# Kernel optimization log

Hardware: AMD Instinct MI355X
Metric: run time of the kernel (lower is better)

Reference implementation:

```python
import jax, jax.numpy as jnp
import numpy as np

EPS = 1e-5

def _ln(x, w, b):
    m = jnp.mean(x, -1, keepdims=True)
    v = jnp.mean((x - m) ** 2, -1, keepdims=True)
    return (x - m) * jax.lax.rsqrt(v + EPS) * w + b

def _silu(x):
    return x * jax.nn.sigmoid(x)

def _mamba(x, in_proj_w, conv_w, conv_b, x_proj_w, dt_proj_w, dt_proj_b, A_log, D, out_proj_w):
    # x: [Bc, L, d_model]; standard mamba_ssm Mamba block math
    Bc, L, _ = x.shape
    d_inner = conv_b.shape[0]
    d_state = A_log.shape[1]
    dt_rank = dt_proj_w.shape[0]
    xz = x @ in_proj_w                          # [Bc, L, 2*d_inner]
    xm, z = jnp.split(xz, 2, axis=-1)
    # causal depthwise conv1d (pad left d_conv-1, truncate to L)
    xm_t = jnp.transpose(xm, (0, 2, 1))         # [Bc, d_inner, L]
    xm_t = jax.lax.conv_general_dilated(
        xm_t, conv_w[:, None, :], (1,), [(conv_w.shape[-1] - 1, 0)],
        dimension_numbers=('NCH', 'OIH', 'NCH'), feature_group_count=d_inner)
    xm = _silu(jnp.transpose(xm_t, (0, 2, 1)) + conv_b)   # [Bc, L, d_inner]
    x_dbl = xm @ x_proj_w                        # [Bc, L, dt_rank + 2*d_state]
    dt_r = x_dbl[..., :dt_rank]
    Bm = x_dbl[..., dt_rank:dt_rank + d_state]
    Cm = x_dbl[..., dt_rank + d_state:]
    dt = jax.nn.softplus(dt_r @ dt_proj_w + dt_proj_b)    # [Bc, L, d_inner]
    A = -jnp.exp(A_log)                          # [d_inner, d_state]

    def step(h, inp):
        xt, dtt, Bt, Ct = inp                    # [Bc,d_inner],[Bc,d_inner],[Bc,d_state],[Bc,d_state]
        dA = jnp.exp(dtt[:, :, None] * A)
        h = dA * h + (dtt * xt)[:, :, None] * Bt[:, None, :]
        y = jnp.einsum('bds,bs->bd', h, Ct)
        return h, y

    h0 = jnp.zeros((Bc, d_inner, d_state), x.dtype)
    xs = (jnp.transpose(xm, (1, 0, 2)), jnp.transpose(dt, (1, 0, 2)),
          jnp.transpose(Bm, (1, 0, 2)), jnp.transpose(Cm, (1, 0, 2)))
    _, ys = jax.lax.scan(step, h0, xs)
    y = jnp.transpose(ys, (1, 0, 2)) + xm * D    # [Bc, L, d_inner]
    y = y * _silu(z)
    return y @ out_proj_w                        # [Bc, L, d_model]

def _pvmamba(x, ln_w, ln_b, skip_scale, proj_w, proj_b, mp):
    # x: [B, H, W, C]; 4 channel-chunks share one Mamba -> batch them as lanes
    B, H, W, C = x.shape
    n = H * W
    d = C // 4
    xf = x.reshape(B, n, C)
    xn = _ln(xf, ln_w, ln_b)
    xc = jnp.transpose(xn.reshape(B, n, 4, d), (2, 0, 1, 3)).reshape(4 * B, n, d)
    ym = _mamba(xc, *mp) + skip_scale * xc
    ym = jnp.transpose(ym.reshape(4, B, n, d), (1, 2, 0, 3)).reshape(B, n, C)
    ym = _ln(ym, ln_w, ln_b)                     # second LN reuses same params (as in source)
    out = ym @ proj_w + proj_b
    return out.reshape(B, H, W, -1)

def _down(x, w):
    # Conv2d k=2 s=2 no bias, exact non-overlapping patch contraction; w: [O, I, 2, 2]
    B, H, W, C = x.shape
    xr = jnp.transpose(x, (0, 3, 1, 2)).reshape(B, C, H // 2, 2, W // 2, 2)
    y = jnp.einsum('bcipjq,ocpq->boij', xr, w)
    return jnp.transpose(y, (0, 2, 3, 1))

def _up(x, w):
    # ConvTranspose2d k=2 s=2 no bias; w: [I, O, 2, 2] (torch layout)
    B, H, W, C = x.shape
    xc = jnp.transpose(x, (0, 3, 1, 2))
    y = jnp.einsum('bcij,copq->boipjq', xc, w).reshape(B, w.shape[1], 2 * H, 2 * W)
    return jnp.transpose(y, (0, 2, 3, 1))

def _mpma(x, ln_w, ln_b, skip_scale, proj_w, proj_b, in_proj_w, conv_w, conv_b,
          x_proj_w, dt_proj_w, dt_proj_b, A_log, D, out_proj_w, down_w, up_w):
    mp = (in_proj_w, conv_w, conv_b, x_proj_w, dt_proj_w, dt_proj_b, A_log, D, out_proj_w)
    xh = jnp.transpose(x, (0, 2, 3, 1))          # NCHW -> NHWC
    outs = [_pvmamba(xh, ln_w, ln_b, skip_scale, proj_w, proj_b, mp)]
    xin = xh
    for _ in range(1, 5):
        xin = _down(xin, down_w)
        outs.append(_pvmamba(xin, ln_w, ln_b, skip_scale, proj_w, proj_b, mp))
    res = outs[-1]
    for l, od in enumerate(outs[-2::-1]):
        res = od + (1.0 / (l + 1)) * _up(res, up_w)
    return jnp.transpose(res, (0, 3, 2, 1))      # note: (0,3,2,1) as in source -> [B,C,W,H]

def setup_inputs() -> dict:
    B, C, HW = 8, 64, 128
    d_model, d_inner, d_state, d_conv, dt_rank = 16, 32, 16, 4, 1
    key = jax.random.key(0)
    ks = jax.random.split(key, 10)
    x = jax.random.normal(ks[0], (B, C, HW, HW), jnp.float32)
    return {
        'x': x,
        'ln_w': jnp.ones((C,), jnp.float32),
        'ln_b': jnp.zeros((C,), jnp.float32),
        'skip_scale': jnp.ones((1,), jnp.float32),
        'proj_w': jax.random.normal(ks[1], (C, C), jnp.float32) * 0.05,
        'proj_b': jnp.zeros((C,), jnp.float32),
        'in_proj_w': jax.random.normal(ks[2], (d_model, 2 * d_inner), jnp.float32) * 0.1,
        'conv_w': jax.random.normal(ks[3], (d_inner, d_conv), jnp.float32) * 0.2,
        'conv_b': jnp.zeros((d_inner,), jnp.float32),
        'x_proj_w': jax.random.normal(ks[4], (d_inner, dt_rank + 2 * d_state), jnp.float32) * 0.1,
        'dt_proj_w': jax.random.normal(ks[5], (dt_rank, d_inner), jnp.float32) * 0.5,
        'dt_proj_b': jnp.full((d_inner,), -4.0, jnp.float32),
        'A_log': jnp.broadcast_to(jnp.log(jnp.arange(1, d_state + 1, dtype=jnp.float32)), (d_inner, d_state)),
        'D': jnp.ones((d_inner,), jnp.float32),
        'out_proj_w': jax.random.normal(ks[6], (d_inner, d_model), jnp.float32) * 0.1,
        'down_w': jax.random.normal(ks[7], (C, C, 2, 2), jnp.float32) * 0.05,
        'up_w': jax.random.normal(ks[8], (C, C, 2, 2), jnp.float32) * 0.05,
    }

def reference(x, ln_w, ln_b, skip_scale, proj_w, proj_b, in_proj_w, conv_w, conv_b,
              x_proj_w, dt_proj_w, dt_proj_b, A_log, D, out_proj_w, down_w, up_w):
    return _mpma(x, ln_w, ln_b, skip_scale, proj_w, proj_b, in_proj_w, conv_w, conv_b,
                 x_proj_w, dt_proj_w, dt_proj_b, A_log, D, out_proj_w, down_w, up_w)
```

## Files before the change

kernel.cpp:

```cpp
#include <hip/hip_runtime.h>
#include <hip/hip_fp16.h>

#define TMAX 128

__device__ __forceinline__ float silu_f(float x) {
    return x / (1.f + __expf(-x));
}
__device__ __forceinline__ float softplus_f(float x) {
    return (x > 20.f) ? x : log1pf(__expf(x));
}

__global__ __launch_bounds__(256) void k_tr_in(const float* __restrict__ x, float* __restrict__ xh) {
    __shared__ float tile[128 * 65];
    int h = blockIdx.x, b = blockIdx.y;
    const float* ip = x + (size_t)b * 64 * 16384 + (size_t)h * 128;
    for (int i = threadIdx.x; i < 64 * 128; i += 256) {
        int c = i >> 7, w = i & 127;
        tile[w * 65 + c] = ip[(size_t)c * 16384 + w];
    }
    __syncthreads();
    float* op = xh + ((size_t)(b * 128 + h)) * 128 * 64;
    for (int i = threadIdx.x; i < 128 * 64; i += 256) {
        int w = i >> 6, c = i & 63;
        op[i] = tile[w * 65 + c];
    }
}

__global__ __launch_bounds__(256) void k_tr_out(const float* __restrict__ res, float* __restrict__ out) {
    __shared__ float tile[64 * 129];
    int w = blockIdx.x, b = blockIdx.y;
    const float* ip = res + (size_t)b * 16384 * 64 + (size_t)w * 64;
    for (int i = threadIdx.x; i < 128 * 64; i += 256) {
        int h = i >> 6, c = i & 63;
        tile[c * 129 + h] = ip[(size_t)h * 128 * 64 + c];
    }
    __syncthreads();
    float* op = out + (size_t)b * 64 * 16384 + (size_t)w * 128;
    for (int i = threadIdx.x; i < 64 * 128; i += 256) {
        int c = i >> 7, hh = i & 127;
        op[(size_t)c * 16384 + hh] = tile[c * 129 + hh];
    }
}

__global__ __launch_bounds__(256) void k_down(const float* __restrict__ in, float* __restrict__ out,
                                              const float* __restrict__ dwp, int Ho, int Wo, int ntot) {
    __shared__ float dw[16384];
    for (int i = threadIdx.x; i < 16384; i += 256) {
        int o = i & 63, cpq = i >> 6;
        dw[cpq * 64 + o] = dwp[o * 256 + cpq];
    }
    __syncthreads();
    int gid = blockIdx.x * 256 + threadIdx.x;
    if (gid >= ntot) return;
    int og = gid & 3, pix = gid >> 2;
    int j = pix % Wo, i2 = (pix / Wo) % Ho, b = pix / (Wo * Ho);
    const float* ip = in + (((size_t)b * (2 * Ho) + 2 * i2) * (size_t)(2 * Wo) + 2 * j) * 64;
    float acc[16];
#pragma unroll
    for (int m = 0; m < 16; ++m) acc[m] = 0.f;
    for (int p = 0; p < 2; ++p) {
        for (int q = 0; q < 2; ++q) {
            const float* xp = ip + ((size_t)p * (2 * Wo) + q) * 64;
            for (int c = 0; c < 64; ++c) {
                float xv = xp[c];
                const float* wrow = &dw[(c * 4 + p * 2 + q) * 64 + og * 16];
#pragma unroll
                for (int m = 0; m < 16; ++m) acc[m] = fmaf(xv, wrow[m], acc[m]);
            }
        }
    }
    float* op = out + (size_t)pix * 64 + og * 16;
#pragma unroll
    for (int m = 0; m < 4; ++m) {
        float4 v = make_float4(acc[m * 4], acc[m * 4 + 1], acc[m * 4 + 2], acc[m * 4 + 3]);
        *(float4*)(op + m * 4) = v;
    }
}

__global__ __launch_bounds__(256) void k_up(const float* __restrict__ src, float* __restrict__ dst,
                                            const float* __restrict__ uwp, int H, int W, float coef, int ntot) {
    __shared__ float uw[16384];
    for (int i = threadIdx.x; i < 16384; i += 256) {
        int o = i & 63, cpq = i >> 6;
        int c = cpq >> 2, pq = cpq & 3;
        uw[cpq * 64 + o] = uwp[c * 256 + o * 4 + pq];
    }
    __syncthreads();
    int gid = blockIdx.x * 256 + threadIdx.x;
    if (gid >= ntot) return;
    int og = gid & 3, pix = gid >> 2;
    int x = pix % W, y = (pix / W) % H, b = pix / (W * H);
    int Hs = H >> 1, Ws = W >> 1;
    int pq = (y & 1) * 2 + (x & 1);
    const float* sp = src + (((size_t)b * Hs + (y >> 1)) * (size_t)Ws + (x >> 1)) * 64;
    float acc[16];
#pragma unroll
    for (int m = 0; m < 16; ++m) acc[m] = 0.f;
    for (int c = 0; c < 64; ++c) {
        float xv = sp[c];
        const float* wrow = &uw[(c * 4 + pq) * 64 + og * 16];
#pragma unroll
        for (int m = 0; m < 16; ++m) acc[m] = fmaf(xv, wrow[m], acc[m]);
    }
    float* op = dst + (size_t)pix * 64 + og * 16;
#pragma unroll
    for (int m = 0; m < 4; ++m) {
        float4 cur = *(float4*)(op + m * 4);
        cur.x += coef * acc[m * 4];
        cur.y += coef * acc[m * 4 + 1];
        cur.z += coef * acc[m * 4 + 2];
        cur.w += coef * acc[m * 4 + 3];
        *(float4*)(op + m * 4) = cur;
    }
}

__global__ __launch_bounds__(256) void k_pre(const float* __restrict__ xh, __half2* __restrict__ stream,
                                             const float* __restrict__ lnw, const float* __restrict__ lnb,
                                             const float* __restrict__ in_proj_w, const float* __restrict__ conv_w,
                                             const float* __restrict__ conv_b, const float* __restrict__ x_proj_w,
                                             const float* __restrict__ dt_w, const float* __restrict__ dt_b,
                                             int n, int nseq, int seq_base) {
    __shared__ float pre[259][33];
    __shared__ float Wm[16][32];
    __shared__ float Wxp[32][33];
    __shared__ float cw[32][4];
    __shared__ float cb[32], dtw[32], dtb[32];
    __shared__ float lw[64], lb[64];
    const int tid = threadIdx.x;
    const int t0 = blockIdx.x * 256;
    const int seqL = blockIdx.y;
    const int seqG = seq_base + seqL;
    const int b = seqG >> 2, g = seqG & 3;

    for (int i = tid; i < 512; i += 256) Wm[i >> 5][i & 31] = in_proj_w[(i >> 5) * 64 + (i & 31)];
    for (int i = tid; i < 32 * 33; i += 256) Wxp[i / 33][i % 33] = x_proj_w[i];
    for (int i = tid; i < 128; i += 256) cw[i >> 2][i & 3] = conv_w[i];
    if (tid < 32) { cb[tid] = conv_b[tid]; dtw[tid] = dt_w[tid]; dtb[tid] = dt_b[tid]; }
    if (tid < 64) { lw[tid] = lnw[tid]; lb[tid] = lnb[tid]; }
    __syncthreads();

    const int Tcb = min(256, n - t0);
    const int rows = Tcb + 3;
    for (int r = tid; r < rows; r += 256) {
        int t = t0 + r - 3;
        if (t < 0) {
#pragma unroll
            for (int d = 0; d < 32; ++d) pre[r][d] = 0.f;
        } else {
            const float4* xp = (const float4*)(xh + ((size_t)b * n + t) * 64);
            float4 v[16];
            float s = 0.f;
#pragma unroll
            for (int i = 0; i < 16; ++i) { v[i] = xp[i]; s += v[i].x + v[i].y + v[i].z + v[i].w; }
            float m = s * (1.f / 64.f);
            float q = 0.f;
#pragma unroll
            for (int i = 0; i < 16; ++i) {
                float a = v[i].x - m, b2 = v[i].y - m, c = v[i].z - m, dd = v[i].w - m;
                q += a * a + b2 * b2 + c * c + dd * dd;
            }
            float rr = rsqrtf(q * (1.f / 64.f) + 1e-5f);
            const float4* xg = (const float4*)(xh + ((size_t)b * n + t) * 64 + g * 16);
            float xn16[16];
#pragma unroll
            for (int i = 0; i < 4; ++i) {
                float4 u4 = xg[i];
                int c0 = g * 16 + i * 4;
                xn16[i * 4 + 0] = (u4.x - m) * rr * lw[c0 + 0] + lb[c0 + 0];
                xn16[i * 4 + 1] = (u4.y - m) * rr * lw[c0 + 1] + lb[c0 + 1];
                xn16[i * 4 + 2] = (u4.z - m) * rr * lw[c0 + 2] + lb[c0 + 2];
                xn16[i * 4 + 3] = (u4.w - m) * rr * lw[c0 + 3] + lb[c0 + 3];
            }
#pragma unroll
            for (int d = 0; d < 32; ++d) {
                float a = 0.f;
#pragma unroll
                for (int j = 0; j < 16; ++j) a = fmaf(xn16[j], Wm[j][d], a);
                pre[r][d] = a;
            }
        }
    }
    __syncthreads();

    if (tid < Tcb) {
        const int t = t0 + tid;
        float xmv[32];
#pragma unroll
        for (int d = 0; d < 32; ++d) {
            float a = cb[d];
#pragma unroll
            for (int k = 0; k < 4; ++k) a = fmaf(pre[tid + k][d], cw[d][k], a);
            xmv[d] = silu_f(a);
        }
        float dtr = 0.f;
#pragma unroll
        for (int d = 0; d < 32; ++d) dtr = fmaf(xmv[d], Wxp[d][0], dtr);
        const size_t sb = (size_t)seqL * n + t;
#pragma unroll
        for (int d = 0; d < 32; ++d) {
            float dtv = softplus_f(fmaf(dtr, dtw[d], dtb[d]));
            stream[(size_t)d * nseq * n + sb] = __floats2half2_rn(dtv, xmv[d]);
        }
#pragma unroll
        for (int p = 0; p < 8; ++p) {
            float b0 = 0.f, b1 = 0.f;
#pragma unroll
            for (int d = 0; d < 32; ++d) {
                b0 = fmaf(xmv[d], Wxp[d][1 + 2 * p], b0);
                b1 = fmaf(xmv[d], Wxp[d][2 + 2 * p], b1);
            }
            stream[(size_t)(32 + p) * nseq * n + sb] = __floats2half2_rn(b0, b1);
        }
#pragma unroll
        for (int p = 0; p < 8; ++p) {
            float c0 = 0.f, c1 = 0.f;
#pragma unroll
            for (int d = 0; d < 32; ++d) {
                c0 = fmaf(xmv[d], Wxp[d][17 + 2 * p], c0);
                c1 = fmaf(xmv[d], Wxp[d][18 + 2 * p], c1);
            }
            stream[(size_t)(40 + p) * nseq * n + sb] = __floats2half2_rn(c0, c1);
        }
    }
}

__global__ __launch_bounds__(256) void k_scanA(const __half2* __restrict__ stream, float* __restrict__ P,
                                               float* __restrict__ H, const float* __restrict__ A_log,
                                               int n, int nseq, int nch) {
    const int tid = threadIdx.x;
    const int d = tid >> 3, ss = tid & 7;
    const int chunk = blockIdx.x, seqL = blockIdx.y;
    const int t0 = chunk * TMAX;
    const int Tc = min(TMAX, n - t0);
    const float a0 = -__expf(A_log[d * 16 + 2 * ss]);
    const float a1 = -__expf(A_log[d * 16 + 2 * ss + 1]);
    const __half2* pdx = stream + ((size_t)d * nseq + seqL) * n + t0;
    const __half2* pB = stream + ((size_t)(32 + ss) * nseq + seqL) * n + t0;
    float h0 = 0.f, h1 = 0.f, sdt = 0.f;
    for (int t = 0; t < Tc; ++t) {
        float2 dx = __half22float2(pdx[t]);
        float2 bv = __half22float2(pB[t]);
        float u = dx.x * dx.y;
        h0 = fmaf(__expf(a0 * dx.x), h0, u * bv.x);
        h1 = fmaf(__expf(a1 * dx.x), h1, u * bv.y);
        sdt += dx.x;
    }
    const size_t cbi = ((size_t)seqL * nch + chunk) * 512 + tid * 2;
    *(float2*)&P[cbi] = make_float2(__expf(a0 * sdt), __expf(a1 * sdt));
    *(float2*)&H[cbi] = make_float2(h0, h1);
}

__global__ __launch_bounds__(256) void k_scanB(const float* __restrict__ P, const float* __restrict__ Hl,
                                               float* __restrict__ hin, int nch, int nseq) {
    int idx = blockIdx.x * 256 + threadIdx.x;
    if (idx >= nseq * 512) return;
    int seq = idx >> 9, ds = idx & 511;
    size_t base = (size_t)seq * nch * 512 + ds;
    float h = 0.f;
    for (int k = 0; k < nch; ++k) {
        hin[base + (size_t)k * 512] = h;
        h = fmaf(P[base + (size_t)k * 512], h, Hl[base + (size_t)k * 512]);
    }
}

__global__ __launch_bounds__(256) void k_scanC(const __half2* __restrict__ stream, const float* __restrict__ hin,
                                               const float* __restrict__ xh, float* __restrict__ ym,
                                               const float* __restrict__ A_log,
                                               const float* __restrict__ lnw, const float* __restrict__ lnb,
                                               const float* __restrict__ in_proj_w, const float* __restrict__ Dvec,
                                               const float* __restrict__ out_proj_w,
                                               const float* __restrict__ skip_scale,
                                               int n, int nseq, int seq_base, int nch) {
    __shared__ float yb[TMAX][33];
    __shared__ float Wz[16][32];
    __shared__ float Wout[32][16];
    __shared__ float lw[64], lb[64];
    __shared__ float Dsh[32];
    const int tid = threadIdx.x;
    const int d = tid >> 3, ss = tid & 7;
    const int chunk = blockIdx.x, seqL = blockIdx.y;
    const int seqG = seq_base + seqL;
    const int b = seqG >> 2, g = seqG & 3;
    const int t0 = chunk * TMAX;
    const int Tc = min(TMAX, n - t0);

    for (int i = tid; i < 512; i += 256) Wz[i >> 5][i & 31] = in_proj_w[(i >> 5) * 64 + 32 + (i & 31)];
    for (int i = tid; i < 512; i += 256) Wout[i >> 4][i & 15] = out_proj_w[i];
    if (tid < 64) { lw[tid] = lnw[tid]; lb[tid] = lnb[tid]; }
    if (tid < 32) Dsh[tid] = Dvec[tid];

    const float a0 = -__expf(A_log[d * 16 + 2 * ss]);
    const float a1 = -__expf(A_log[d * 16 + 2 * ss + 1]);
    const __half2* pdx = stream + ((size_t)d * nseq + seqL) * n + t0;
    const __half2* pB = stream + ((size_t)(32 + ss) * nseq + seqL) * n + t0;
    const __half2* pC = stream + ((size_t)(40 + ss) * nseq + seqL) * n + t0;
    const size_t cbi = ((size_t)seqL * nch + chunk) * 512 + tid * 2;
    float2 hi2 = *(const float2*)&hin[cbi];
    float h0 = hi2.x, h1 = hi2.y;

    for (int t = 0; t < Tc; ++t) {
        float2 dx = __half22float2(pdx[t]);
        float2 bv = __half22float2(pB[t]);
        float2 cv = __half22float2(pC[t]);
        float u = dx.x * dx.y;
        h0 = fmaf(__expf(a0 * dx.x), h0, u * bv.x);
        h1 = fmaf(__expf(a1 * dx.x), h1, u * bv.y);
        float pp = fmaf(h0, cv.x, h1 * cv.y);
        pp += __shfl_xor(pp, 1);
        pp += __shfl_xor(pp, 2);
        pp += __shfl_xor(pp, 4);
        if (ss == 0) yb[t][d] = pp;
    }
    __syncthreads();

    if (tid < Tc) {
        const int t = t0 + tid;
        const float4* xp = (const float4*)(xh + ((size_t)b * n + t) * 64);
        float4 v[16];
        float s = 0.f;
#pragma unroll
        for (int i = 0; i < 16; ++i) { v[i] = xp[i]; s += v[i].x + v[i].y + v[i].z + v[i].w; }
        float m = s * (1.f / 64.f);
        float q = 0.f;
#pragma unroll
        for (int i = 0; i < 16; ++i) {
            float a = v[i].x - m, b2 = v[i].y - m, c = v[i].z - m, dd = v[i].w - m;
            q += a * a + b2 * b2 + c * c + dd * dd;
        }
        float rr = rsqrtf(q * (1.f / 64.f) + 1e-5f);
        const float4* xg = (const float4*)(xh + ((size_t)b * n + t) * 64 + g * 16);
        float xc[16];
#pragma unroll
        for (int i = 0; i < 4; ++i) {
            float4 u4 = xg[i];
            int c0 = g * 16 + i * 4;
            xc[i * 4 + 0] = (u4.x - m) * rr * lw[c0 + 0] + lb[c0 + 0];
            xc[i * 4 + 1] = (u4.y - m) * rr * lw[c0 + 1] + lb[c0 + 1];
            xc[i * 4 + 2] = (u4.z - m) * rr * lw[c0 + 2] + lb[c0 + 2];
            xc[i * 4 + 3] = (u4.w - m) * rr * lw[c0 + 3] + lb[c0 + 3];
        }
        float yv[32];
#pragma unroll
        for (int dd = 0; dd < 32; ++dd) {
            float2 dx = __half22float2(stream[((size_t)dd * nseq + seqL) * n + t0 + tid]);
            float zz = 0.f;
#pragma unroll
            for (int j = 0; j < 16; ++j) zz = fmaf(xc[j], Wz[j][dd], zz);
            yv[dd] = (yb[tid][dd] + dx.y * Dsh[dd]) * silu_f(zz);
        }
        float sscale = skip_scale[0];
        float* ymtok = ym + ((size_t)b * n + t) * 64 + g * 16;
#pragma unroll
        for (int jq = 0; jq < 4; ++jq) {
            float o0 = 0.f, o1 = 0.f, o2 = 0.f, o3 = 0.f;
#pragma unroll
            for (int dd = 0; dd < 32; ++dd) {
                o0 = fmaf(yv[dd], Wout[dd][jq * 4 + 0], o0);
                o1 = fmaf(yv[dd], Wout[dd][jq * 4 + 1], o1);
                o2 = fmaf(yv[dd], Wout[dd][jq * 4 + 2], o2);
                o3 = fmaf(yv[dd], Wout[dd][jq * 4 + 3], o3);
            }
            float4 ov = make_float4(o0 + sscale * xc[jq * 4 + 0], o1 + sscale * xc[jq * 4 + 1],
                                    o2 + sscale * xc[jq * 4 + 2], o3 + sscale * xc[jq * 4 + 3]);
            *(float4*)(ymtok + jq * 4) = ov;
        }
    }
}

__global__ __launch_bounds__(256) void k_post(const float* __restrict__ ym, float* __restrict__ outl,
                                              const float* __restrict__ lnw, const float* __restrict__ lnb,
                                              const float* __restrict__ proj_w, const float* __restrict__ proj_b,
                                              int ntok) {
    __shared__ float pw[4096];
    __shared__ float pb[64];
    __shared__ float lw[64], lb[64];
    for (int i = threadIdx.x; i < 4096; i += 256) pw[i] = proj_w[i];
    if (threadIdx.x < 64) {
        pb[threadIdx.x] = proj_b[threadIdx.x];
        lw[threadIdx.x] = lnw[threadIdx.x];
        lb[threadIdx.x] = lnb[threadIdx.x];
    }
    __syncthreads();
    int t = blockIdx.x * 256 + threadIdx.x;
    if (t >= ntok) return;
    const float4* p = (const float4*)(ym + (size_t)t * 64);
    float4 v[16];
    float s = 0.f;
#pragma unroll
    for (int i = 0; i < 16; ++i) {
        v[i] = p[i];
        s += v[i].x + v[i].y + v[i].z + v[i].w;
    }
    float m = s * (1.f / 64.f);
    float q = 0.f;
#pragma unroll
    for (int i = 0; i < 16; ++i) {
        float a = v[i].x - m, b2 = v[i].y - m, c = v[i].z - m, d = v[i].w - m;
        q += a * a + b2 * b2 + c * c + d * d;
    }
    float r = rsqrtf(q * (1.f / 64.f) + 1e-5f);
    float* op = outl + (size_t)t * 64;
    for (int half = 0; half < 2; ++half) {
        float acc[32];
#pragma unroll
        for (int o = 0; o < 32; ++o) acc[o] = pb[half * 32 + o];
#pragma unroll
        for (int i = 0; i < 16; ++i) {
            float vals[4] = {v[i].x, v[i].y, v[i].z, v[i].w};
#pragma unroll
            for (int k = 0; k < 4; ++k) {
                int c = i * 4 + k;
                float vn = (vals[k] - m) * r * lw[c] + lb[c];
                const float* wrow = &pw[c * 64 + half * 32];
#pragma unroll
                for (int o = 0; o < 32; ++o) acc[o] = fmaf(vn, wrow[o], acc[o]);
            }
        }
#pragma unroll
        for (int mq = 0; mq < 8; ++mq) {
            float4 ov = make_float4(acc[mq * 4], acc[mq * 4 + 1], acc[mq * 4 + 2], acc[mq * 4 + 3]);
            *(float4*)(op + half * 32 + mq * 4) = ov;
        }
    }
}

extern "C" void kernel_launch(void* const* d_in, const int* in_sizes, int n_in,
                              void* d_out, int out_size, void* d_ws, size_t ws_size,
                              hipStream_t stream_) {
    (void)in_sizes; (void)n_in; (void)out_size;
    const float* x          = (const float*)d_in[0];
    const float* ln_w       = (const float*)d_in[1];
    const float* ln_b       = (const float*)d_in[2];
    const float* skip_scale = (const float*)d_in[3];
    const float* proj_w     = (const float*)d_in[4];
    const float* proj_b     = (const float*)d_in[5];
    const float* in_proj_w  = (const float*)d_in[6];
    const float* conv_w     = (const float*)d_in[7];
    const float* conv_b     = (const float*)d_in[8];
    const float* x_proj_w   = (const float*)d_in[9];
    const float* dt_proj_w  = (const float*)d_in[10];
    const float* dt_proj_b  = (const float*)d_in[11];
    const float* A_log      = (const float*)d_in[12];
    const float* Dv         = (const float*)d_in[13];
    const float* out_proj_w = (const float*)d_in[14];
    const float* down_w     = (const float*)d_in[15];
    const float* up_w       = (const float*)d_in[16];
    float* out = (float*)d_out;
    float* ws = (float*)d_ws;

    static const int nl[5] = {16384, 4096, 1024, 256, 64};
    static const size_t off_xh[5] = {0, 8388608, 10485760, 11010048, 11141120};
    const size_t OFF_YM = 11173888;
    static const size_t off_out[5] = {19562496, 27951104, 30048256, 30572544, 30703616};
    const size_t OFF_P = 30736384, OFF_H = 32833536, OFF_HIN = 34930688;
    const size_t STR_BYTE_OFF = 37027840ULL * 4ULL;
    __half2* strm = (__half2*)((char*)d_ws + STR_BYTE_OFF);

    k_tr_in<<<dim3(128, 8), dim3(256), 0, stream_>>>(x, ws + off_xh[0]);

    for (int l = 0; l < 4; ++l) {
        int Ho = 128 >> (l + 1);
        int ntot = 8 * Ho * Ho * 4;
        k_down<<<dim3((ntot + 255) / 256), dim3(256), 0, stream_>>>(ws + off_xh[l], ws + off_xh[l + 1],
                                                                    down_w, Ho, Ho, ntot);
    }

    for (int l = 0; l < 5; ++l) {
        int n = nl[l];
        int ntok = 8 * n;
        int nch = (n + TMAX - 1) / TMAX;
        int nblk = (n + 255) / 256;
        int Sl = 1;
        while (Sl < 32 && STR_BYTE_OFF + (size_t)192 * (32 / Sl) * n > ws_size) Sl <<= 1;
        int nseq = 32 / Sl;
        for (int sp = 0; sp < Sl; ++sp) {
            int sb = sp * nseq;
            k_pre<<<dim3(nblk, nseq), dim3(256), 0, stream_>>>(ws + off_xh[l], strm, ln_w, ln_b, in_proj_w,
                                                               conv_w, conv_b, x_proj_w, dt_proj_w, dt_proj_b,
                                                               n, nseq, sb);
            k_scanA<<<dim3(nch, nseq), dim3(256), 0, stream_>>>(strm, ws + OFF_P, ws + OFF_H, A_log, n, nseq, nch);
            k_scanB<<<dim3(nseq * 2), dim3(256), 0, stream_>>>(ws + OFF_P, ws + OFF_H, ws + OFF_HIN, nch, nseq);
            k_scanC<<<dim3(nch, nseq), dim3(256), 0, stream_>>>(strm, ws + OFF_HIN, ws + off_xh[l], ws + OFF_YM,
                                                                A_log, ln_w, ln_b, in_proj_w, Dv, out_proj_w,
                                                                skip_scale, n, nseq, sb, nch);
        }
        k_post<<<dim3((ntok + 255) / 256), dim3(256), 0, stream_>>>(ws + OFF_YM, ws + off_out[l], ln_w, ln_b,
                                                                    proj_w, proj_b, ntok);
    }

    static const float coefs[4] = {1.f, 0.5f, 1.f / 3.f, 0.25f};
    for (int k = 0; k < 4; ++k) {
        int l = 3 - k;
        int H = 128 >> l;
        int ntot = 8 * H * H * 4;
        k_up<<<dim3((ntot + 255) / 256), dim3(256), 0, stream_>>>(ws + off_out[l + 1], ws + off_out[l],
                                                                  up_w, H, H, coefs[k], ntot);
    }

    k_tr_out<<<dim3(128, 8), dim3(256), 0, stream_>>>(ws + off_out[0], out);
}
```

Before: 1.654 ms.

## Switch scan stream to token-major records and remap scan threads per sequence

```diff
diff --git a/kernel.cpp b/kernel.cpp
--- a/kernel.cpp
+++ b/kernel.cpp
@@ -1,7 +1,7 @@
 #include <hip/hip_runtime.h>
 #include <hip/hip_fp16.h>
 
-#define TMAX 128
+#define TCH 64
 
 __device__ __forceinline__ float silu_f(float x) {
     return x / (1.f + __expf(-x));
@@ -114,7 +114,7 @@
     }
 }
 
-__global__ __launch_bounds__(256) void k_pre(const float* __restrict__ xh, __half2* __restrict__ stream,
+__global__ __launch_bounds__(256) void k_pre(const float* __restrict__ xh, char* __restrict__ stream,
                                              const float* __restrict__ lnw, const float* __restrict__ lnb,
                                              const float* __restrict__ in_proj_w, const float* __restrict__ conv_w,
                                              const float* __restrict__ conv_b, const float* __restrict__ x_proj_w,
@@ -160,11 +160,10 @@
                 q += a * a + b2 * b2 + c * c + dd * dd;
             }
             float rr = rsqrtf(q * (1.f / 64.f) + 1e-5f);
-            const float4* xg = (const float4*)(xh + ((size_t)b * n + t) * 64 + g * 16);
             float xn16[16];
 #pragma unroll
             for (int i = 0; i < 4; ++i) {
-                float4 u4 = xg[i];
+                float4 u4 = xp[g * 4 + i];
                 int c0 = g * 16 + i * 4;
                 xn16[i * 4 + 0] = (u4.x - m) * rr * lw[c0 + 0] + lb[c0 + 0];
                 xn16[i * 4 + 1] = (u4.y - m) * rr * lw[c0 + 1] + lb[c0 + 1];
@@ -195,11 +194,11 @@
         float dtr = 0.f;
 #pragma unroll
         for (int d = 0; d < 32; ++d) dtr = fmaf(xmv[d], Wxp[d][0], dtr);
-        const size_t sb = (size_t)seqL * n + t;
+        __half2 hbuf[48];
 #pragma unroll
         for (int d = 0; d < 32; ++d) {
             float dtv = softplus_f(fmaf(dtr, dtw[d], dtb[d]));
-            stream[(size_t)d * nseq * n + sb] = __floats2half2_rn(dtv, xmv[d]);
+            hbuf[d] = __floats2half2_rn(dtv, xmv[d]);
         }
 #pragma unroll
         for (int p = 0; p < 8; ++p) {
@@ -209,7 +208,7 @@
                 b0 = fmaf(xmv[d], Wxp[d][1 + 2 * p], b0);
                 b1 = fmaf(xmv[d], Wxp[d][2 + 2 * p], b1);
             }
-            stream[(size_t)(32 + p) * nseq * n + sb] = __floats2half2_rn(b0, b1);
+            hbuf[32 + p] = __floats2half2_rn(b0, b1);
         }
 #pragma unroll
         for (int p = 0; p < 8; ++p) {
@@ -219,35 +218,52 @@
                 c0 = fmaf(xmv[d], Wxp[d][17 + 2 * p], c0);
                 c1 = fmaf(xmv[d], Wxp[d][18 + 2 * p], c1);
             }
-            stream[(size_t)(40 + p) * nseq * n + sb] = __floats2half2_rn(c0, c1);
-        }
-    }
-}
-
-__global__ __launch_bounds__(256) void k_scanA(const __half2* __restrict__ stream, float* __restrict__ P,
+            hbuf[40 + p] = __floats2half2_rn(c0, c1);
+        }
+        float4* o = (float4*)(stream + ((size_t)seqL * n + t) * 192);
+        const float4* src = (const float4*)hbuf;
+#pragma unroll
+        for (int i = 0; i < 12; ++i) o[i] = src[i];
+    }
+}
+
+__global__ __launch_bounds__(256) void k_scanA(const char* __restrict__ stream, float* __restrict__ P,
                                                float* __restrict__ H, const float* __restrict__ A_log,
                                                int n, int nseq, int nch) {
     const int tid = threadIdx.x;
-    const int d = tid >> 3, ss = tid & 7;
-    const int chunk = blockIdx.x, seqL = blockIdx.y;
-    const int t0 = chunk * TMAX;
-    const int Tc = min(TMAX, n - t0);
-    const float a0 = -__expf(A_log[d * 16 + 2 * ss]);
-    const float a1 = -__expf(A_log[d * 16 + 2 * ss + 1]);
-    const __half2* pdx = stream + ((size_t)d * nseq + seqL) * n + t0;
-    const __half2* pB = stream + ((size_t)(32 + ss) * nseq + seqL) * n + t0;
-    float h0 = 0.f, h1 = 0.f, sdt = 0.f;
-    for (int t = 0; t < Tc; ++t) {
-        float2 dx = __half22float2(pdx[t]);
-        float2 bv = __half22float2(pB[t]);
+    const int wv = tid >> 6, lane = tid & 63;
+    const int d = lane & 31, hh = lane >> 5;
+    const int chunk = blockIdx.x;
+    const int seqL = blockIdx.y * 4 + wv;
+    if (seqL >= nseq) return;
+    const char* rec = stream + ((size_t)seqL * n + (size_t)chunk * TCH) * 192;
+    float Av[8];
+#pragma unroll
+    for (int j = 0; j < 8; ++j) Av[j] = -__expf(A_log[d * 16 + hh * 8 + j]);
+    float hs[8] = {0.f, 0.f, 0.f, 0.f, 0.f, 0.f, 0.f, 0.f};
+    float sdt = 0.f;
+    for (int t = 0; t < TCH; ++t) {
+        const char* r = rec + t * 192;
+        float2 dx = __half22float2(*(const __half2*)(r + d * 4));
+        float4 bv4 = *(const float4*)(r + 128 + hh * 16);
+        const __half2* bh = (const __half2*)&bv4;
         float u = dx.x * dx.y;
-        h0 = fmaf(__expf(a0 * dx.x), h0, u * bv.x);
-        h1 = fmaf(__expf(a1 * dx.x), h1, u * bv.y);
+#pragma unroll
+        for (int j = 0; j < 4; ++j) {
+            float2 bf = __half22float2(bh[j]);
+            hs[2 * j]     = fmaf(__expf(Av[2 * j] * dx.x),     hs[2 * j],     u * bf.x);
+            hs[2 * j + 1] = fmaf(__expf(Av[2 * j + 1] * dx.x), hs[2 * j + 1], u * bf.y);
+        }
         sdt += dx.x;
     }
-    const size_t cbi = ((size_t)seqL * nch + chunk) * 512 + tid * 2;
-    *(float2*)&P[cbi] = make_float2(__expf(a0 * sdt), __expf(a1 * sdt));
-    *(float2*)&H[cbi] = make_float2(h0, h1);
+    size_t base = ((size_t)seqL * nch + chunk) * 512 + d * 16 + hh * 8;
+    float pv[8];
+#pragma unroll
+    for (int j = 0; j < 8; ++j) pv[j] = __expf(Av[j] * sdt);
+    *(float4*)&P[base]     = *(float4*)&pv[0];
+    *(float4*)&P[base + 4] = *(float4*)&pv[4];
+    *(float4*)&H[base]     = *(float4*)&hs[0];
+    *(float4*)&H[base + 4] = *(float4*)&hs[4];
 }
 
 __global__ __launch_bounds__(256) void k_scanB(const float* __restrict__ P, const float* __restrict__ Hl,
@@ -263,7 +279,7 @@
     }
 }
 
-__global__ __launch_bounds__(256) void k_scanC(const __half2* __restrict__ stream, const float* __restrict__ hin,
+__global__ __launch_bounds__(256) void k_scanC(const char* __restrict__ stream, const float* __restrict__ hin,
                                                const float* __restrict__ xh, float* __restrict__ ym,
                                                const float* __restrict__ A_log,
                                                const float* __restrict__ lnw, const float* __restrict__ lnb,
@@ -271,50 +287,61 @@
                                                const float* __restrict__ out_proj_w,
                                                const float* __restrict__ skip_scale,
                                                int n, int nseq, int seq_base, int nch) {
-    __shared__ float yb[TMAX][33];
+    __shared__ float yb[4][TCH][33];
     __shared__ float Wz[16][32];
     __shared__ float Wout[32][16];
     __shared__ float lw[64], lb[64];
-    __shared__ float Dsh[32];
     const int tid = threadIdx.x;
-    const int d = tid >> 3, ss = tid & 7;
-    const int chunk = blockIdx.x, seqL = blockIdx.y;
-    const int seqG = seq_base + seqL;
-    const int b = seqG >> 2, g = seqG & 3;
-    const int t0 = chunk * TMAX;
-    const int Tc = min(TMAX, n - t0);
-
     for (int i = tid; i < 512; i += 256) Wz[i >> 5][i & 31] = in_proj_w[(i >> 5) * 64 + 32 + (i & 31)];
     for (int i = tid; i < 512; i += 256) Wout[i >> 4][i & 15] = out_proj_w[i];
     if (tid < 64) { lw[tid] = lnw[tid]; lb[tid] = lnb[tid]; }
-    if (tid < 32) Dsh[tid] = Dvec[tid];
-
-    const float a0 = -__expf(A_log[d * 16 + 2 * ss]);
-    const float a1 = -__expf(A_log[d * 16 + 2 * ss + 1]);
-    const __half2* pdx = stream + ((size_t)d * nseq + seqL) * n + t0;
-    const __half2* pB = stream + ((size_t)(32 + ss) * nseq + seqL) * n + t0;
-    const __half2* pC = stream + ((size_t)(40 + ss) * nseq + seqL) * n + t0;
-    const size_t cbi = ((size_t)seqL * nch + chunk) * 512 + tid * 2;
-    float2 hi2 = *(const float2*)&hin[cbi];
-    float h0 = hi2.x, h1 = hi2.y;
-
-    for (int t = 0; t < Tc; ++t) {
-        float2 dx = __half22float2(pdx[t]);
-        float2 bv = __half22float2(pB[t]);
-        float2 cv = __half22float2(pC[t]);
-        float u = dx.x * dx.y;
-        h0 = fmaf(__expf(a0 * dx.x), h0, u * bv.x);
-        h1 = fmaf(__expf(a1 * dx.x), h1, u * bv.y);
-        float pp = fmaf(h0, cv.x, h1 * cv.y);
-        pp += __shfl_xor(pp, 1);
-        pp += __shfl_xor(pp, 2);
-        pp += __shfl_xor(pp, 4);
-        if (ss == 0) yb[t][d] = pp;
-    }
-    __syncthreads();
-
-    if (tid < Tc) {
-        const int t = t0 + tid;
+    __syncthreads();
+
+    const int wv = tid >> 6, lane = tid & 63;
+    const int d = lane & 31, hh = lane >> 5;
+    const int chunk = blockIdx.x;
+    const int t0 = chunk * TCH;
+    const int seqL = blockIdx.y * 4 + wv;
+
+    if (seqL < nseq) {
+        const char* rec = stream + ((size_t)seqL * n + (size_t)t0) * 192;
+        float Av[8];
+#pragma unroll
+        for (int j = 0; j < 8; ++j) Av[j] = -__expf(A_log[d * 16 + hh * 8 + j]);
+        const float Dd = Dvec[d];
+        size_t base = ((size_t)seqL * nch + chunk) * 512 + d * 16 + hh * 8;
+        float hs[8];
+        *(float4*)&hs[0] = *(const float4*)&hin[base];
+        *(float4*)&hs[4] = *(const float4*)&hin[base + 4];
+        for (int t = 0; t < TCH; ++t) {
+            const char* r = rec + t * 192;
+            float2 dx = __half22float2(*(const __half2*)(r + d * 4));
+            float4 bv4 = *(const float4*)(r + 128 + hh * 16);
+            float4 cv4 = *(const float4*)(r + 160 + hh * 16);
+            const __half2* bh = (const __half2*)&bv4;
+            const __half2* ch = (const __half2*)&cv4;
+            float u = dx.x * dx.y;
+            float pp = 0.f;
+#pragma unroll
+            for (int j = 0; j < 4; ++j) {
+                float2 bf = __half22float2(bh[j]);
+                float2 cf = __half22float2(ch[j]);
+                hs[2 * j]     = fmaf(__expf(Av[2 * j] * dx.x),     hs[2 * j],     u * bf.x);
+                hs[2 * j + 1] = fmaf(__expf(Av[2 * j + 1] * dx.x), hs[2 * j + 1], u * bf.y);
+                pp = fmaf(hs[2 * j], cf.x, pp);
+                pp = fmaf(hs[2 * j + 1], cf.y, pp);
+            }
+            pp += __shfl_xor(pp, 32);
+            if (hh == 0) yb[wv][t][d] = fmaf(dx.y, Dd, pp);
+        }
+    }
+    __syncthreads();
+
+    const int tl = tid & 63;
+    if (seqL < nseq) {
+        const int seqG = seq_base + seqL;
+        const int b = seqG >> 2, g = seqG & 3;
+        const int t = t0 + tl;
         const float4* xp = (const float4*)(xh + ((size_t)b * n + t) * 64);
         float4 v[16];
         float s = 0.f;
@@ -328,11 +355,10 @@
             q += a * a + b2 * b2 + c * c + dd * dd;
         }
         float rr = rsqrtf(q * (1.f / 64.f) + 1e-5f);
-        const float4* xg = (const float4*)(xh + ((size_t)b * n + t) * 64 + g * 16);
         float xc[16];
 #pragma unroll
         for (int i = 0; i < 4; ++i) {
-            float4 u4 = xg[i];
+            float4 u4 = v[g * 4 + i];
             int c0 = g * 16 + i * 4;
             xc[i * 4 + 0] = (u4.x - m) * rr * lw[c0 + 0] + lb[c0 + 0];
             xc[i * 4 + 1] = (u4.y - m) * rr * lw[c0 + 1] + lb[c0 + 1];
@@ -342,11 +368,10 @@
         float yv[32];
 #pragma unroll
         for (int dd = 0; dd < 32; ++dd) {
-            float2 dx = __half22float2(stream[((size_t)dd * nseq + seqL) * n + t0 + tid]);
             float zz = 0.f;
 #pragma unroll
             for (int j = 0; j < 16; ++j) zz = fmaf(xc[j], Wz[j][dd], zz);
-            yv[dd] = (yb[tid][dd] + dx.y * Dsh[dd]) * silu_f(zz);
+            yv[dd] = yb[wv][tl][dd] * silu_f(zz);
         }
         float sscale = skip_scale[0];
         float* ymtok = ym + ((size_t)b * n + t) * 64 + g * 16;
@@ -367,7 +392,7 @@
     }
 }
 
-__global__ __launch_bounds__(256) void k_post(const float* __restrict__ ym, float* __restrict__ outl,
+__global__ __launch_bounds__(256) void k_post(float* buf,
                                               const float* __restrict__ lnw, const float* __restrict__ lnb,
                                               const float* __restrict__ proj_w, const float* __restrict__ proj_b,
                                               int ntok) {
@@ -383,7 +408,7 @@
     __syncthreads();
     int t = blockIdx.x * 256 + threadIdx.x;
     if (t >= ntok) return;
-    const float4* p = (const float4*)(ym + (size_t)t * 64);
+    const float4* p = (const float4*)(buf + (size_t)t * 64);
     float4 v[16];
     float s = 0.f;
 #pragma unroll
@@ -399,7 +424,8 @@
         q += a * a + b2 * b2 + c * c + d * d;
     }
     float r = rsqrtf(q * (1.f / 64.f) + 1e-5f);
-    float* op = outl + (size_t)t * 64;
+    float* op = buf + (size_t)t * 64;
+    float outv[64];
     for (int half = 0; half < 2; ++half) {
         float acc[32];
 #pragma unroll
@@ -417,10 +443,12 @@
             }
         }
 #pragma unroll
-        for (int mq = 0; mq < 8; ++mq) {
-            float4 ov = make_float4(acc[mq * 4], acc[mq * 4 + 1], acc[mq * 4 + 2], acc[mq * 4 + 3]);
-            *(float4*)(op + half * 32 + mq * 4) = ov;
-        }
+        for (int o = 0; o < 32; ++o) outv[half * 32 + o] = acc[o];
+    }
+#pragma unroll
+    for (int mq = 0; mq < 16; ++mq) {
+        float4 ov = make_float4(outv[mq * 4], outv[mq * 4 + 1], outv[mq * 4 + 2], outv[mq * 4 + 3]);
+        *(float4*)(op + mq * 4) = ov;
     }
 }
 
@@ -449,12 +477,11 @@
     float* ws = (float*)d_ws;
 
     static const int nl[5] = {16384, 4096, 1024, 256, 64};
-    static const size_t off_xh[5] = {0, 8388608, 10485760, 11010048, 11141120};
-    const size_t OFF_YM = 11173888;
-    static const size_t off_out[5] = {19562496, 27951104, 30048256, 30572544, 30703616};
-    const size_t OFF_P = 30736384, OFF_H = 32833536, OFF_HIN = 34930688;
-    const size_t STR_BYTE_OFF = 37027840ULL * 4ULL;
-    __half2* strm = (__half2*)((char*)d_ws + STR_BYTE_OFF);
+    static const size_t off_xh[5]  = {0, 8388608, 10485760, 11010048, 11141120};
+    static const size_t off_out[5] = {11173888, 19562496, 21659648, 22183936, 22315008};
+    const size_t OFF_P = 22347776, OFF_H = 26542080, OFF_HIN = 30736384;
+    const size_t STR_BYTE_OFF = 34930688ULL * 4ULL;
+    char* strm = (char*)d_ws + STR_BYTE_OFF;
 
     k_tr_in<<<dim3(128, 8), dim3(256), 0, stream_>>>(x, ws + off_xh[0]);
 
@@ -468,23 +495,25 @@
     for (int l = 0; l < 5; ++l) {
         int n = nl[l];
         int ntok = 8 * n;
-        int nch = (n + TMAX - 1) / TMAX;
+        int nch = n / TCH;
         int nblk = (n + 255) / 256;
         int Sl = 1;
-        while (Sl < 32 && STR_BYTE_OFF + (size_t)192 * (32 / Sl) * n > ws_size) Sl <<= 1;
+        while (Sl < 32 && STR_BYTE_OFF + (size_t)192 * (size_t)(32 / Sl) * (size_t)n > ws_size) Sl <<= 1;
         int nseq = 32 / Sl;
+        int gy = (nseq + 3) / 4;
         for (int sp = 0; sp < Sl; ++sp) {
             int sb = sp * nseq;
             k_pre<<<dim3(nblk, nseq), dim3(256), 0, stream_>>>(ws + off_xh[l], strm, ln_w, ln_b, in_proj_w,
                                                                conv_w, conv_b, x_proj_w, dt_proj_w, dt_proj_b,
                                                                n, nseq, sb);
-            k_scanA<<<dim3(nch, nseq), dim3(256), 0, stream_>>>(strm, ws + OFF_P, ws + OFF_H, A_log, n, nseq, nch);
-            k_scanB<<<dim3(nseq * 2), dim3(256), 0, stream_>>>(ws + OFF_P, ws + OFF_H, ws + OFF_HIN, nch, nseq);
-            k_scanC<<<dim3(nch, nseq), dim3(256), 0, stream_>>>(strm, ws + OFF_HIN, ws + off_xh[l], ws + OFF_YM,
-                                                                A_log, ln_w, ln_b, in_proj_w, Dv, out_proj_w,
-                                                                skip_scale, n, nseq, sb, nch);
-        }
-        k_post<<<dim3((ntok + 255) / 256), dim3(256), 0, stream_>>>(ws + OFF_YM, ws + off_out[l], ln_w, ln_b,
+            k_scanA<<<dim3(nch, gy), dim3(256), 0, stream_>>>(strm, ws + OFF_P, ws + OFF_H, A_log, n, nseq, nch);
+            k_scanB<<<dim3((nseq * 512 + 255) / 256), dim3(256), 0, stream_>>>(ws + OFF_P, ws + OFF_H,
+                                                                               ws + OFF_HIN, nch, nseq);
+            k_scanC<<<dim3(nch, gy), dim3(256), 0, stream_>>>(strm, ws + OFF_HIN, ws + off_xh[l], ws + off_out[l],
+                                                              A_log, ln_w, ln_b, in_proj_w, Dv, out_proj_w,
+                                                              skip_scale, n, nseq, sb, nch);
+        }
+        k_post<<<dim3((ntok + 255) / 256), dim3(256), 0, stream_>>>(ws + off_out[l], ln_w, ln_b,
                                                                     proj_w, proj_b, ntok);
     }
 
```

Measured after the change: 1.719 ms. +3.9%, slower.
